# Optimization experiments

Measured on AMD Instinct MI355X. Metric: run time of the kernel, lower is better.

## Reference

```python
import jax, jax.numpy as jnp
import numpy as np
from jax import lax

R = 128            # grid resolution (full-depth N3Tree equivalent)
BASIS = 9          # SH degree 2 -> 9 basis functions
DATA_DIM = 3 * BASIS + 1
B = 262144         # rays (512x512 image)
STEP_SIZE = 0.001
BG = 1.0           # background_brightness
NUM_STEPS = 256    # >= sqrt(3)*R worst-case voxel crossings

SH_C0 = 0.28209479177387814
SH_C1 = 0.4886025119029199
SH_C2 = (1.0925484305920792, -1.0925484305920792, 0.31539156525252005,
         -1.0925484305920792, 0.5462742152960396)


def eval_sh_bases(d):
    # d: [B,3] unit view directions -> [B,9] SH deg-2 basis values (matches svox.sh)
    x, y, z = d[:, 0], d[:, 1], d[:, 2]
    return jnp.stack([
        jnp.full_like(x, SH_C0),
        -SH_C1 * y,
        SH_C1 * z,
        -SH_C1 * x,
        SH_C2[0] * x * y,
        SH_C2[1] * y * z,
        SH_C2[2] * (2.0 * z * z - x * x - y * y),
        SH_C2[3] * x * z,
        SH_C2[4] * (x * x - y * y),
    ], axis=-1)


def dda_unit(cen, invdir):
    # slab intersection of ray (cen + t*dir) with unit cube [0,1]^3
    t1 = -cen * invdir            # [B,3]
    t2 = t1 + invdir
    tmin = jnp.maximum(jnp.max(jnp.minimum(t1, t2), axis=-1), 0.0)
    tmax = jnp.minimum(jnp.min(jnp.maximum(t1, t2), axis=-1), 1e9)
    return tmin, tmax


def setup_inputs() -> dict:
    key = jax.random.key(0)
    k1, k2, k3, k4 = jax.random.split(key, 4)
    origins = jax.random.uniform(k1, (B, 3), jnp.float32, 0.05, 0.95)
    dirs = jax.random.normal(k2, (B, 3), jnp.float32)
    viewdirs = jax.random.normal(k3, (B, 3), jnp.float32)
    viewdirs = viewdirs / jnp.linalg.norm(viewdirs, axis=-1, keepdims=True)
    tree_data = jax.random.normal(k4, (R, R, R, DATA_DIM), jnp.float32) * 0.5
    invradius = jnp.ones((3,), jnp.float32)
    return {"tree_data": tree_data, "origins": origins, "dirs": dirs,
            "viewdirs": viewdirs, "invradius": invradius}


def _render(tree_data, origins, dirs, viewdirs, invradius):
    nb = origins.shape[0]
    dirs = dirs / jnp.linalg.norm(dirs, axis=-1, keepdims=True)
    sh_mult = eval_sh_bases(viewdirs)[:, None, :]          # [B,1,9]
    invdirs = 1.0 / (dirs + 1e-9)
    t0, tmax = dda_unit(origins, invdirs)
    delta_scale = jnp.linalg.norm(dirs / invradius[None], axis=-1)  # [B]
    grid = tree_data.reshape(R * R * R, DATA_DIM)
    cube_sz = 1.0 / R

    def step(carry, _):
        t, light, out, active = carry
        pos = origins + t[:, None] * dirs                  # [B,3] in tree coords
        idx = jnp.clip(jnp.floor(pos * R), 0.0, R - 1.0)
        flat = (idx[:, 0] * (R * R) + idx[:, 1] * R + idx[:, 2]).astype(jnp.int32)
        rgba = grid[flat]                                  # [B,28] voxel query
        pos_t = pos * R - idx                              # local coords in voxel
        s0, s1 = dda_unit(pos_t, invdirs)
        dt = (s1 - s0) * cube_sz + STEP_SIZE
        sigma = jax.nn.relu(rgba[:, -1])
        att = jnp.exp(-dt * sigma * delta_scale)
        weight = light * (1.0 - att)
        rgb_sh = rgba[:, :-1].reshape(-1, 3, BASIS)
        rgb = jax.nn.sigmoid(jnp.sum(sh_mult * rgb_sh, axis=-1))  # [B,3]
        am = active[:, None]
        out = out + jnp.where(am, weight[:, None] * rgb, 0.0)
        light = jnp.where(active, light * att, light)
        t = t + jnp.where(active, dt, 0.0)
        active = active & (t < tmax)
        return (t, light, out, active), None

    init = (t0, jnp.ones((nb,), jnp.float32), jnp.zeros((nb, 3), jnp.float32),
            t0 < tmax)
    (t, light, out, active), _ = lax.scan(step, init, None, length=NUM_STEPS)
    # remaining transmittance hits background (white by default)
    return out + light[:, None] * BG


def reference(tree_data, origins, dirs, viewdirs, invradius):
    return _render(tree_data, origins, dirs, viewdirs, invradius)
```

## Files before the change

kernel.cpp:

```cpp
#include <hip/hip_runtime.h>
#include <hip/hip_fp16.h>
#include <math.h>

#define GRID_R 128
#define DATA_DIM 28
#define PAD_DIM 32
#define NSEG 8
#define SEG_STEPS 32
#define STEP_SIZE 0.001f
#define BG 1.0f

typedef _Float16 h2f __attribute__((ext_vector_type(2)));

#if __has_builtin(__builtin_amdgcn_fdot2)
__device__ __forceinline__ float fdot2(h2f a, h2f b, float c) {
    return __builtin_amdgcn_fdot2(a, b, c, false);
}
#else
__device__ __forceinline__ float fdot2(h2f a, h2f b, float c) {
    return fmaf((float)a.x, (float)b.x, fmaf((float)a.y, (float)b.y, c));
}
#endif

#if __has_builtin(__builtin_amdgcn_exp2f)
__device__ __forceinline__ float fexp2(float x)    { return __builtin_amdgcn_exp2f(x); }
__device__ __forceinline__ float fexp2neg(float x) { return __builtin_amdgcn_exp2f(-x); }
#else
__device__ __forceinline__ float fexp2(float x) {
    float r; asm("v_exp_f32 %0, %1" : "=v"(r) : "v"(x)); return r;
}
__device__ __forceinline__ float fexp2neg(float x) {
    float r; asm("v_exp_f32 %0, -%1" : "=v"(r) : "v"(x)); return r;
}
#endif

#if __has_builtin(__builtin_amdgcn_rcpf)
__device__ __forceinline__ float frcp(float x) { return __builtin_amdgcn_rcpf(x); }
#else
__device__ __forceinline__ float frcp(float x) {
    float r; asm("v_rcp_f32 %0, %1" : "=v"(r) : "v"(x)); return r;
}
#endif

__device__ __forceinline__ float march_step(
    float t, float ox, float oy, float oz,
    float dx, float dy, float dz,
    float idx, float idy, float idz, int* flat)
{
    float px = (ox + t*dx) * 128.0f;
    float py = (oy + t*dy) * 128.0f;
    float pz = (oz + t*dz) * 128.0f;
    float fx = fminf(fmaxf(floorf(px), 0.0f), 127.0f);
    float fy = fminf(fmaxf(floorf(py), 0.0f), 127.0f);
    float fz = fminf(fmaxf(floorf(pz), 0.0f), 127.0f);
    float ff = fmaf(fx, 16384.0f, fmaf(fy, 128.0f, fz));
    *flat = (int)ff;
    float cx = px - fx, cy = py - fy, cz = pz - fz;
    float a1x = -cx*idx, a1y = -cy*idy, a1z = -cz*idz;
    float a2x = a1x+idx, a2y = a1y+idy, a2z = a1z+idz;
    float e1 = fminf(fminf(fmaxf(a1x,a2x), fmaxf(a1y,a2y)), fmaxf(a1z,a2z));
    e1 = fminf(e1, 1e9f);
    return e1 * (1.0f/128.0f) + STEP_SIZE;
}

#define RAY_SETUP(i)                                                          \
    float ox = origins[3*(i)+0], oy = origins[3*(i)+1], oz = origins[3*(i)+2];\
    float dx = dirs_in[3*(i)+0], dy = dirs_in[3*(i)+1], dz = dirs_in[3*(i)+2];\
    float dn = sqrtf(dx*dx + dy*dy + dz*dz);                                  \
    float rdn = 1.0f / dn;                                                    \
    dx *= rdn; dy *= rdn; dz *= rdn;                                          \
    float idx = 1.0f / (dx + 1e-9f);                                          \
    float idy = 1.0f / (dy + 1e-9f);                                          \
    float idz = 1.0f / (dz + 1e-9f);                                          \
    float t1x = -ox*idx, t1y = -oy*idy, t1z = -oz*idz;                        \
    float t2x = t1x+idx, t2y = t1y+idy, t2z = t1z+idz;                        \
    float t0   = fmaxf(fmaxf(fmaxf(fminf(t1x,t2x), fminf(t1y,t2y)), fminf(t1z,t2z)), 0.0f); \
    float tmax = fminf(fminf(fminf(fmaxf(t1x,t2x), fmaxf(t1y,t2y)), fmaxf(t1z,t2z)), 1e9f);

__global__ __launch_bounds__(256) void prep_kernel(
    const float* __restrict__ tree, __half* __restrict__ vox, int nvox,
    const float* __restrict__ origins, const float* __restrict__ dirs_in,
    float* __restrict__ ckpt, unsigned char* __restrict__ occ_mask,
    int nB, int nGeomB, int nConvB)
{
    int bid = (int)blockIdx.x;
    if (bid < nGeomB) {
        int i = bid * 256 + threadIdx.x;
        if (i >= nB) return;
        RAY_SETUP(i);
        float ck[NSEG];
        float t = t0;
        ck[0] = t0;
#pragma unroll
        for (int k = 1; k < NSEG; ++k) {
            if (t < tmax) {
                for (int j = 0; j < SEG_STEPS; ++j) {
                    int fl;
                    t += march_step(t, ox, oy, oz, dx, dy, dz, idx, idy, idz, &fl);
                    if (t >= tmax) break;
                }
            }
            ck[k] = t;
        }
        float* cp = ckpt + (size_t)i * NSEG;
        *(float4*)(cp + 0) = make_float4(ck[0], ck[1], ck[2], ck[3]);
        *(float4*)(cp + 4) = make_float4(ck[4], ck[5], ck[6], ck[7]);
    } else if (bid < nGeomB + nConvB) {
        int tid2 = (bid - nGeomB) * 256 + threadIdx.x;
        int v = tid2 >> 1;
        int q = tid2 & 1;
        if (v >= nvox) return;
        const float* src = tree + (size_t)v * DATA_DIM;
        uint4* d = (uint4*)(vox + (size_t)v * PAD_DIM) + q * 2;
        union Q { __half2 h[4]; uint4 u; } w;
        if (q == 0) {
            float4 L0 = *(const float4*)(src + 0);
            float4 L1 = *(const float4*)(src + 4);
            float4 L2 = *(const float4*)(src + 8);
            float4 L3 = *(const float4*)(src + 12);
            w.h[0] = __floats2half2_rn(L0.x, L0.y);
            w.h[1] = __floats2half2_rn(L0.z, L0.w);
            w.h[2] = __floats2half2_rn(L1.x, L1.y);
            w.h[3] = __floats2half2_rn(L1.z, L1.w);
            d[0] = w.u;
            w.h[0] = __floats2half2_rn(L2.x, 0.f);
            w.h[1] = __floats2half2_rn(L2.y, L2.z);
            w.h[2] = __floats2half2_rn(L2.w, L3.x);
            w.h[3] = __floats2half2_rn(L3.y, L3.z);
            d[1] = w.u;
        } else {
            float4 M0 = *(const float4*)(src + 12);
            float4 M1 = *(const float4*)(src + 16);
            float4 M2 = *(const float4*)(src + 20);
            float4 M3 = *(const float4*)(src + 24);
            w.h[0] = __floats2half2_rn(M0.w, M1.x);
            w.h[1] = __floats2half2_rn(M1.y, 0.f);
            w.h[2] = __floats2half2_rn(M1.z, M1.w);
            w.h[3] = __floats2half2_rn(M2.x, M2.y);
            d[0] = w.u;
            w.h[0] = __floats2half2_rn(M2.z, M2.w);
            w.h[1] = __floats2half2_rn(M3.x, M3.y);
            w.h[2] = __floats2half2_rn(M3.z, 0.f);
            w.h[3] = __floats2half2_rn(M3.w, 0.f);
            d[1] = w.u;
        }
    } else {
        int m = (bid - nGeomB - nConvB) * 256 + threadIdx.x;
        int nm = nvox >> 3;
        if (m >= nm) return;
        const float* s = tree + (size_t)m * 8 * DATA_DIM + (DATA_DIM - 1);
        unsigned int b = 0;
#pragma unroll
        for (int j = 0; j < 8; ++j)
            if (s[(size_t)j * DATA_DIM] > 0.0f) b |= (1u << j);
        occ_mask[m] = (unsigned char)b;
    }
}

typedef union { uint4 u[4]; h2f h[16]; _Float16 s[32]; } Rec;

__global__ __launch_bounds__(256, 8) void march_kernel(
    const __half* __restrict__ vox_grid,
    const unsigned char* __restrict__ occ_mask,
    const float* __restrict__ origins,
    const float* __restrict__ dirs_in,
    const float* __restrict__ viewdirs,
    const float* __restrict__ invradius,
    const float* __restrict__ ckpt,
    float* __restrict__ out, int nB)
{
    int tid = blockIdx.x * blockDim.x + threadIdx.x;
    int ray = tid >> 3;
    int seg = tid & 7;
    if (ray >= nB) return;

    RAY_SETUP(ray);

    float vx = viewdirs[3*ray+0], vy = viewdirs[3*ray+1], vz = viewdirs[3*ray+2];
    float irx = invradius[0], iry = invradius[1], irz = invradius[2];
    float qx = dx / irx, qy = dy / iry, qz = dz / irz;
    float delta_scale = sqrtf(qx*qx + qy*qy + qz*qz);

    const float C1 = 0.4886025119029199f;
    const float L2E = 1.4426950408889634f;
    float sh0 = 0.28209479177387814f;
    float sh1 = -C1 * vy;
    float sh2 =  C1 * vz;
    float sh3 = -C1 * vx;
    float sh4 =  1.0925484305920792f  * vx * vy;
    float sh5 = -1.0925484305920792f * vy * vz;
    float sh6 =  0.31539156525252005f * (2.0f*vz*vz - vx*vx - vy*vy);
    float sh7 = -1.0925484305920792f * vx * vz;
    float sh8 =  0.5462742152960396f  * (vx*vx - vy*vy);

    h2f S01 = { (_Float16)(sh0*L2E), (_Float16)(sh1*L2E) };
    h2f S23 = { (_Float16)(sh2*L2E), (_Float16)(sh3*L2E) };
    h2f S45 = { (_Float16)(sh4*L2E), (_Float16)(sh5*L2E) };
    h2f S67 = { (_Float16)(sh6*L2E), (_Float16)(sh7*L2E) };
    h2f S8z = { (_Float16)(sh8*L2E), (_Float16)0.0f      };
    float nds = -delta_scale * L2E;

    float t = ckpt[(size_t)ray * NSEG + seg];
    float light = 1.0f;
    float o0 = 0.f, o1 = 0.f, o2 = 0.f;

    for (int j = 0; j < SEG_STEPS; ++j) {
        if (t >= tmax) break;
        int flat;
        float dt = march_step(t, ox, oy, oz, dx, dy, dz, idx, idy, idz, &flat);

        unsigned int mb = occ_mask[flat >> 3];
        if (mb & (1u << (flat & 7))) {
            const uint4* vp = (const uint4*)(vox_grid + (size_t)flat * PAD_DIM);
            Rec rec;
            rec.u[0] = vp[0]; rec.u[1] = vp[1];
            rec.u[2] = vp[2]; rec.u[3] = vp[3];

            float sigma = (float)rec.s[30];
            float att = fexp2(dt * sigma * nds);
            float la  = light * att;
            float w   = light - la;
            light = la;

            float r0 = fdot2(rec.h[ 4], S8z, fdot2(rec.h[ 3], S67,
                       fdot2(rec.h[ 2], S45, fdot2(rec.h[ 1], S23,
                       fdot2(rec.h[ 0], S01, 0.0f)))));
            float r1 = fdot2(rec.h[ 9], S8z, fdot2(rec.h[ 8], S67,
                       fdot2(rec.h[ 7], S45, fdot2(rec.h[ 6], S23,
                       fdot2(rec.h[ 5], S01, 0.0f)))));
            float r2 = fdot2(rec.h[14], S8z, fdot2(rec.h[13], S67,
                       fdot2(rec.h[12], S45, fdot2(rec.h[11], S23,
                       fdot2(rec.h[10], S01, 0.0f)))));

            float g0 = frcp(1.0f + fexp2neg(r0));
            float g1 = frcp(1.0f + fexp2neg(r1));
            float g2 = frcp(1.0f + fexp2neg(r2));

            o0 = fmaf(w, g0, o0);
            o1 = fmaf(w, g1, o1);
            o2 = fmaf(w, g2, o2);
        }
        t += dt;
    }

    float l0 = __shfl(light, 0, 8);
    float l1 = __shfl(light, 1, 8);
    float l2 = __shfl(light, 2, 8);
    float l3 = __shfl(light, 3, 8);
    float l4 = __shfl(light, 4, 8);
    float l5 = __shfl(light, 5, 8);
    float l6 = __shfl(light, 6, 8);
    float l7 = __shfl(light, 7, 8);

    float P = 1.0f;
    if (seg > 0) P *= l0;
    if (seg > 1) P *= l1;
    if (seg > 2) P *= l2;
    if (seg > 3) P *= l3;
    if (seg > 4) P *= l4;
    if (seg > 5) P *= l5;
    if (seg > 6) P *= l6;
    float total_light = l0*l1*l2*l3*l4*l5*l6*l7;

    o0 *= P; o1 *= P; o2 *= P;
    o0 += __shfl_xor(o0, 1, 8); o0 += __shfl_xor(o0, 2, 8); o0 += __shfl_xor(o0, 4, 8);
    o1 += __shfl_xor(o1, 1, 8); o1 += __shfl_xor(o1, 2, 8); o1 += __shfl_xor(o1, 4, 8);
    o2 += __shfl_xor(o2, 1, 8); o2 += __shfl_xor(o2, 2, 8); o2 += __shfl_xor(o2, 4, 8);

    if (seg == 0) {
        out[3*ray+0] = o0 + total_light * BG;
        out[3*ray+1] = o1 + total_light * BG;
        out[3*ray+2] = o2 + total_light * BG;
    }
}

extern "C" void kernel_launch(void* const* d_in, const int* in_sizes, int n_in,
                              void* d_out, int out_size, void* d_ws, size_t ws_size,
                              hipStream_t stream) {
    const float* tree      = (const float*)d_in[0];
    const float* origins   = (const float*)d_in[1];
    const float* dirs      = (const float*)d_in[2];
    const float* viewdirs  = (const float*)d_in[3];
    const float* invradius = (const float*)d_in[4];
    float* out = (float*)d_out;

    int nB   = in_sizes[1] / 3;
    int nvox = in_sizes[0] / DATA_DIM;

    const int block = 256;
    __half* hgrid = (__half*)d_ws;
    float* ckpt = (float*)((char*)d_ws + (size_t)nvox * PAD_DIM * sizeof(__half));
    unsigned char* occ_mask =
        (unsigned char*)((char*)ckpt + (size_t)nB * NSEG * sizeof(float));

    int nGeomB = (nB + block - 1) / block;
    int nConvB = (nvox * 2 + block - 1) / block;
    int nMaskB = ((nvox >> 3) + block - 1) / block;
    prep_kernel<<<nGeomB + nConvB + nMaskB, block, 0, stream>>>(
        tree, hgrid, nvox, origins, dirs, ckpt, occ_mask, nB, nGeomB, nConvB);

    int nmarch = nB * NSEG;
    march_kernel<<<(nmarch + block - 1) / block, block, 0, stream>>>(
        hgrid, occ_mask, origins, dirs, viewdirs, invradius, ckpt, out, nB);
    (void)ws_size;
}
```

Baseline: 641.5 us.

## Replace occupancy bitmask with half-precision sigma array and prefetch next step's sigma

```diff
diff --git a/kernel.cpp b/kernel.cpp
--- a/kernel.cpp
+++ b/kernel.cpp
@@ -80,8 +80,8 @@
 __global__ __launch_bounds__(256) void prep_kernel(
     const float* __restrict__ tree, __half* __restrict__ vox, int nvox,
     const float* __restrict__ origins, const float* __restrict__ dirs_in,
-    float* __restrict__ ckpt, unsigned char* __restrict__ occ_mask,
-    int nB, int nGeomB, int nConvB)
+    float* __restrict__ ckpt, __half* __restrict__ sg_out,
+    int nB, int nGeomB)
 {
     int bid = (int)blockIdx.x;
     if (bid < nGeomB) {
@@ -105,7 +105,7 @@
         float* cp = ckpt + (size_t)i * NSEG;
         *(float4*)(cp + 0) = make_float4(ck[0], ck[1], ck[2], ck[3]);
         *(float4*)(cp + 4) = make_float4(ck[4], ck[5], ck[6], ck[7]);
-    } else if (bid < nGeomB + nConvB) {
+    } else {
         int tid2 = (bid - nGeomB) * 256 + threadIdx.x;
         int v = tid2 >> 1;
         int q = tid2 & 1;
@@ -143,17 +143,8 @@
             w.h[2] = __floats2half2_rn(M3.z, 0.f);
             w.h[3] = __floats2half2_rn(M3.w, 0.f);
             d[1] = w.u;
+            sg_out[v] = __low2half(w.h[3]);
         }
-    } else {
-        int m = (bid - nGeomB - nConvB) * 256 + threadIdx.x;
-        int nm = nvox >> 3;
-        if (m >= nm) return;
-        const float* s = tree + (size_t)m * 8 * DATA_DIM + (DATA_DIM - 1);
-        unsigned int b = 0;
-#pragma unroll
-        for (int j = 0; j < 8; ++j)
-            if (s[(size_t)j * DATA_DIM] > 0.0f) b |= (1u << j);
-        occ_mask[m] = (unsigned char)b;
     }
 }
 
@@ -161,7 +152,7 @@
 
 __global__ __launch_bounds__(256, 8) void march_kernel(
     const __half* __restrict__ vox_grid,
-    const unsigned char* __restrict__ occ_mask,
+    const __half* __restrict__ sig_arr,
     const float* __restrict__ origins,
     const float* __restrict__ dirs_in,
     const float* __restrict__ viewdirs,
@@ -204,20 +195,25 @@
     float light = 1.0f;
     float o0 = 0.f, o1 = 0.f, o2 = 0.f;
 
+    int fA;
+    float dtA = march_step(t, ox, oy, oz, dx, dy, dz, idx, idy, idz, &fA);
+    float sgA = __half2float(sig_arr[fA]);
+
     for (int j = 0; j < SEG_STEPS; ++j) {
         if (t >= tmax) break;
-        int flat;
-        float dt = march_step(t, ox, oy, oz, dx, dy, dz, idx, idy, idz, &flat);
-
-        unsigned int mb = occ_mask[flat >> 3];
-        if (mb & (1u << (flat & 7))) {
-            const uint4* vp = (const uint4*)(vox_grid + (size_t)flat * PAD_DIM);
+
+        float tn = t + dtA;
+        int fB;
+        float dtB = march_step(tn, ox, oy, oz, dx, dy, dz, idx, idy, idz, &fB);
+        float sgB = __half2float(sig_arr[fB]);
+
+        if (sgA > 0.0f) {
+            const uint4* vp = (const uint4*)(vox_grid + (size_t)fA * PAD_DIM);
             Rec rec;
             rec.u[0] = vp[0]; rec.u[1] = vp[1];
             rec.u[2] = vp[2]; rec.u[3] = vp[3];
 
-            float sigma = (float)rec.s[30];
-            float att = fexp2(dt * sigma * nds);
+            float att = fexp2(dtA * sgA * nds);
             float la  = light * att;
             float w   = light - la;
             light = la;
@@ -240,7 +236,8 @@
             o1 = fmaf(w, g1, o1);
             o2 = fmaf(w, g2, o2);
         }
-        t += dt;
+
+        t = tn; fA = fB; dtA = dtB; sgA = sgB;
     }
 
     float l0 = __shfl(light, 0, 8);
@@ -290,17 +287,15 @@
     const int block = 256;
     __half* hgrid = (__half*)d_ws;
     float* ckpt = (float*)((char*)d_ws + (size_t)nvox * PAD_DIM * sizeof(__half));
-    unsigned char* occ_mask =
-        (unsigned char*)((char*)ckpt + (size_t)nB * NSEG * sizeof(float));
+    __half* sgarr = (__half*)((char*)ckpt + (size_t)nB * NSEG * sizeof(float));
 
     int nGeomB = (nB + block - 1) / block;
     int nConvB = (nvox * 2 + block - 1) / block;
-    int nMaskB = ((nvox >> 3) + block - 1) / block;
-    prep_kernel<<<nGeomB + nConvB + nMaskB, block, 0, stream>>>(
-        tree, hgrid, nvox, origins, dirs, ckpt, occ_mask, nB, nGeomB, nConvB);
+    prep_kernel<<<nGeomB + nConvB, block, 0, stream>>>(
+        tree, hgrid, nvox, origins, dirs, ckpt, sgarr, nB, nGeomB);
 
     int nmarch = nB * NSEG;
     march_kernel<<<(nmarch + block - 1) / block, block, 0, stream>>>(
-        hgrid, occ_mask, origins, dirs, viewdirs, invradius, ckpt, out, nB);
+        hgrid, sgarr, origins, dirs, viewdirs, invradius, ckpt, out, nB);
     (void)ws_size;
 }
```

New measurement: 659.7 us. 1.03x slower.
